# Kernel optimization log

Measured on AMD Instinct MI355X. Metric: run time of the kernel, lower is better.

## Reference

```python
import jax, jax.numpy as jnp
import numpy as np

N, D = 8192, 1024
Q = 4096
DK = 512
DV = 256


def setup_inputs() -> dict:
    key = jax.random.key(0)
    k1, k2, k3, k4, k5, k6 = jax.random.split(key, 6)
    return {
        "search_x": jax.random.normal(k1, (N, D), dtype=jnp.float32),
        "search_y": jax.random.normal(k2, (N, DV), dtype=jnp.float32),
        "query_x": jax.random.normal(k3, (Q, D), dtype=jnp.float32),
        "mask": jax.random.randint(k4, (Q, N), 0, 2, dtype=jnp.int64),
        "Wk": jax.random.normal(k5, (D, DK), dtype=jnp.float32) / np.sqrt(D),
        "Wq": jax.random.normal(k6, (D, DK), dtype=jnp.float32) / np.sqrt(D),
    }


def reference(search_x, search_y, query_x, mask, Wk, Wq):
    # key/query modules: bias-free linear projections (n_keys == 1 after _ensure_key_shape)
    keys = search_x @ Wk            # [N, DK]
    qk = query_x @ Wq               # [Q, DK]
    scale = 1.0 / jnp.sqrt(jnp.asarray(DK, dtype=keys.dtype))
    logits = (qk @ keys.T) * scale  # [Q, N]  (== broadcast mul+sum in original)
    # masked softmax over the search dimension (dim=1)
    m = mask > 0                    # [Q, N]
    neg = jnp.finfo(logits.dtype).min
    p = jax.nn.softmax(jnp.where(m, logits, neg), axis=1)
    p = jnp.where(m, p, 0.0)
    # values = noop_value_module(search_x, search_y) = search_y  [N, DV]
    res = p @ search_y              # [Q, DV]
    return res[:, None, :]          # [Q, n_keys=1, DV], matching original output shape
```

## Files before the change

### kernel.cpp

```cpp
#include <hip/hip_runtime.h>
#include <hip/hip_fp16.h>

typedef _Float16 half4v __attribute__((ext_vector_type(4)));
typedef _Float16 half8v __attribute__((ext_vector_type(8)));
typedef float floatx4 __attribute__((ext_vector_type(4)));

#define GLOBAL_AS __attribute__((address_space(1)))
#define LDS_AS __attribute__((address_space(3)))

__device__ __forceinline__ void async_copy16(const _Float16* g, _Float16* l) {
    __builtin_amdgcn_global_load_lds((const GLOBAL_AS unsigned int*)g,
                                     (LDS_AS unsigned int*)l, 16, 0, 0);
}

template <int R>
__device__ __forceinline__ void stage_tile(const _Float16* g, long ldg,
                                           _Float16* lds, int wave, int lane) {
    const int rl = lane >> 3;
    const int gc = (lane & 7) ^ rl;
#pragma unroll
    for (int i = 0; i < (R >> 5); ++i) {
        const int br = wave * (R >> 2) + i * 8;
        async_copy16(g + (long)(br + rl) * ldg + gc * 8, lds + br * 64);
    }
}

__device__ __forceinline__ void tr_tile(const float* __restrict__ in,
                                        _Float16* __restrict__ out, int R, int C,
                                        int br, int bc, int tid, float (*tile)[33]) {
    int tx = tid & 31, ty = tid >> 5;
#pragma unroll
    for (int i = 0; i < 32; i += 8)
        tile[ty + i][tx] = in[(size_t)(br + ty + i) * C + bc + tx];
    __syncthreads();
#pragma unroll
    for (int i = 0; i < 32; i += 8)
        out[(size_t)(bc + ty + i) * R + br + tx] = (_Float16)tile[tx][ty + i];
    __syncthreads();
}

__global__ __launch_bounds__(256) void k_prep(
    const float* __restrict__ search_x, const float* __restrict__ search_y,
    const float* __restrict__ query_x, const int* __restrict__ mask,
    const float* __restrict__ Wk, const float* __restrict__ Wq,
    _Float16* __restrict__ xh, _Float16* __restrict__ qh,
    _Float16* __restrict__ wkT, _Float16* __restrict__ wqT,
    _Float16* __restrict__ yT, unsigned int* __restrict__ bm) {
    __shared__ float tile[32][33];
    const int bx = blockIdx.x, tid = threadIdx.x;
    if (bx < 2048) {
        const int gw = bx * 4 + (tid >> 6);
        const int lane = tid & 63;
        for (int it = 0; it < 64; ++it) {
            const int idx = (gw * 64 + it) * 64 + lane;
            const int v = mask[idx];
            unsigned long long b = __ballot(v > 0);
            if (lane == 0) bm[idx >> 5] = (unsigned int)b;
            if (lane == 32) bm[idx >> 5] = (unsigned int)(b >> 32);
        }
    } else if (bx < 2560) {
        const int base0 = (bx - 2048) * 256 + tid;
        for (int it = 0; it < 16; ++it) {
            const int i = (it * 512 * 256 + base0) * 4;
            float4 v = *(const float4*)(search_x + i);
            half4v h; h[0]=(_Float16)v.x; h[1]=(_Float16)v.y; h[2]=(_Float16)v.z; h[3]=(_Float16)v.w;
            *(half4v*)(xh + i) = h;
        }
    } else if (bx < 2816) {
        const int base0 = (bx - 2560) * 256 + tid;
        for (int it = 0; it < 16; ++it) {
            const int i = (it * 256 * 256 + base0) * 4;
            float4 v = *(const float4*)(query_x + i);
            half4v h; h[0]=(_Float16)v.x; h[1]=(_Float16)v.y; h[2]=(_Float16)v.z; h[3]=(_Float16)v.w;
            *(half4v*)(qh + i) = h;
        }
    } else if (bx < 2944) {
        for (int it = 0; it < 16; ++it) {
            const int t = (bx - 2816) * 16 + it;
            tr_tile(search_y, yT, 8192, 256, (t >> 3) * 32, (t & 7) * 32, tid, tile);
        }
    } else if (bx < 2976) {
        for (int it = 0; it < 16; ++it) {
            const int t = (bx - 2944) * 16 + it;
            tr_tile(Wk, wkT, 1024, 512, (t >> 4) * 32, (t & 15) * 32, tid, tile);
        }
    } else {
        for (int it = 0; it < 16; ++it) {
            const int t = (bx - 2976) * 16 + it;
            tr_tile(Wq, wqT, 1024, 512, (t >> 4) * 32, (t & 15) * 32, tid, tile);
        }
    }
}

__global__ __launch_bounds__(256, 2) void k_proj(const _Float16* __restrict__ xh,
                                                 const _Float16* __restrict__ qh,
                                                 const _Float16* __restrict__ wkT,
                                                 const _Float16* __restrict__ wqT,
                                                 _Float16* __restrict__ keys,
                                                 _Float16* __restrict__ qk) {
    __shared__ __align__(16) _Float16 As[2][128 * 64];
    __shared__ __align__(16) _Float16 Bs[2][128 * 64];
    const int tid = threadIdx.x, lane = tid & 63, wave = tid >> 6;
    const int wm = (wave >> 1) * 64, wn = (wave & 1) * 64;
    const int quad = lane >> 4, lr = lane & 15;
    const bool isK = blockIdx.y < 64;
    const _Float16* A = isK ? xh : qh;
    const _Float16* B = isK ? wkT : wqT;
    _Float16* C = isK ? keys : qk;
    const long m0 = (long)(isK ? blockIdx.y : blockIdx.y - 64) * 128;
    const long n0 = (long)blockIdx.x * 128;

    floatx4 acc[4][4] = {};
    stage_tile<128>(A + m0 * 1024, 1024, As[0], wave, lane);
    stage_tile<128>(B + n0 * 1024, 1024, Bs[0], wave, lane);
    for (int ktI = 0; ktI < 16; ++ktI) {
        __syncthreads();
        const int cb = ktI & 1;
        if (ktI < 15) {
            stage_tile<128>(A + m0 * 1024 + (ktI + 1) * 64, 1024, As[cb ^ 1], wave, lane);
            stage_tile<128>(B + n0 * 1024 + (ktI + 1) * 64, 1024, Bs[cb ^ 1], wave, lane);
        }
#pragma unroll
        for (int kk = 0; kk < 64; kk += 32) {
            const int sl = ((((kk >> 3) + quad) ^ (lr & 7)) * 8);
            half8v af[4], bf[4];
#pragma unroll
            for (int i = 0; i < 4; ++i) af[i] = *(const half8v*)&As[cb][(wm + i * 16 + lr) * 64 + sl];
#pragma unroll
            for (int j = 0; j < 4; ++j) bf[j] = *(const half8v*)&Bs[cb][(wn + j * 16 + lr) * 64 + sl];
#pragma unroll
            for (int i = 0; i < 4; ++i)
#pragma unroll
                for (int j = 0; j < 4; ++j)
                    acc[i][j] = __builtin_amdgcn_mfma_f32_16x16x32_f16(af[i], bf[j], acc[i][j], 0, 0, 0);
        }
    }
#pragma unroll
    for (int i = 0; i < 4; ++i) {
        long rbase = m0 + wm + i * 16 + quad * 4;
#pragma unroll
        for (int j = 0; j < 4; ++j) {
            long col = n0 + wn + j * 16 + lr;
#pragma unroll
            for (int r = 0; r < 4; ++r)
                C[(rbase + r) * 512 + col] = (_Float16)acc[i][j][r];
        }
    }
}

template <int OUT_MODE>
__global__ __launch_bounds__(256) void k_gemm_nt(const _Float16* __restrict__ A,
                                                 const _Float16* __restrict__ B,
                                                 void* __restrict__ C,
                                                 int M, int N, int K, int kChunk,
                                                 float scale) {
    __shared__ __align__(16) _Float16 As[128 * 64];
    __shared__ __align__(16) _Float16 Bs[128 * 64];
    const int tid = threadIdx.x, lane = tid & 63, wave = tid >> 6;
    const int wm = (wave >> 1) * 64, wn = (wave & 1) * 64;
    const int quad = lane >> 4, lr = lane & 15;
    const long m0 = (long)blockIdx.y * 128, n0 = (long)blockIdx.x * 128;
    const int kBegin = blockIdx.z * kChunk;
    const int kEnd   = kBegin + kChunk;

    floatx4 acc[4][4] = {};
    for (int kt = kBegin; kt < kEnd; kt += 64) {
        stage_tile<128>(A + m0 * K + kt, K, As, wave, lane);
        stage_tile<128>(B + n0 * K + kt, K, Bs, wave, lane);
        __syncthreads();
#pragma unroll
        for (int kk = 0; kk < 64; kk += 32) {
            const int sl = ((((kk >> 3) + quad) ^ (lr & 7)) * 8);
            half8v af[4], bf[4];
#pragma unroll
            for (int i = 0; i < 4; ++i) af[i] = *(const half8v*)&As[(wm + i * 16 + lr) * 64 + sl];
#pragma unroll
            for (int j = 0; j < 4; ++j) bf[j] = *(const half8v*)&Bs[(wn + j * 16 + lr) * 64 + sl];
#pragma unroll
            for (int i = 0; i < 4; ++i)
#pragma unroll
                for (int j = 0; j < 4; ++j)
                    acc[i][j] = __builtin_amdgcn_mfma_f32_16x16x32_f16(af[i], bf[j], acc[i][j], 0, 0, 0);
        }
        __syncthreads();
    }
#pragma unroll
    for (int i = 0; i < 4; ++i) {
        long rbase = m0 + wm + i * 16 + quad * 4;
#pragma unroll
        for (int j = 0; j < 4; ++j) {
            long col = n0 + wn + j * 16 + lr;
#pragma unroll
            for (int r = 0; r < 4; ++r) {
                float val = acc[i][j][r] * scale;
                if (OUT_MODE == 0)
                    ((_Float16*)C)[(rbase + r) * (long)N + col] = (_Float16)val;
                else
                    ((float*)C)[(size_t)blockIdx.z * M * N + (rbase + r) * (long)N + col] = val;
            }
        }
    }
}

__global__ __launch_bounds__(256) void k_softmax(_Float16* __restrict__ logits,
                                                 const unsigned int* __restrict__ bm) {
    const int q   = blockIdx.x;
    const int tid = threadIdx.x;
    _Float16* row = logits + (size_t)q * 8192;
    const unsigned int* bmr = bm + (size_t)q * 256;

    float v[32];
    unsigned mb = 0;
    float lmax = -3.0e38f;
#pragma unroll
    for (int i = 0; i < 8; ++i) {
        int base = i * 1024 + tid * 4;
        half4v h = *(const half4v*)(row + base);
        unsigned bits = (bmr[base >> 5] >> ((tid & 7) * 4)) & 0xFu;
#pragma unroll
        for (int j = 0; j < 4; ++j) {
            v[i * 4 + j] = (float)h[j];
            if ((bits >> j) & 1u) {
                mb |= 1u << (i * 4 + j);
                lmax = fmaxf(lmax, v[i * 4 + j]);
            }
        }
    }
#pragma unroll
    for (int off = 32; off > 0; off >>= 1) lmax = fmaxf(lmax, __shfl_xor(lmax, off, 64));
    __shared__ float redmax[4], redsum[4];
    if ((tid & 63) == 0) redmax[tid >> 6] = lmax;
    __syncthreads();
    lmax = fmaxf(fmaxf(redmax[0], redmax[1]), fmaxf(redmax[2], redmax[3]));

    float lsum = 0.f;
#pragma unroll
    for (int i = 0; i < 32; ++i) {
        float e = ((mb >> i) & 1u) ? __expf(v[i] - lmax) : 0.f;
        v[i] = e;
        lsum += e;
    }
#pragma unroll
    for (int off = 32; off > 0; off >>= 1) lsum += __shfl_xor(lsum, off, 64);
    if ((tid & 63) == 0) redsum[tid >> 6] = lsum;
    __syncthreads();
    lsum = redsum[0] + redsum[1] + redsum[2] + redsum[3];
    float inv = lsum > 0.f ? 1.f / lsum : 0.f;

#pragma unroll
    for (int i = 0; i < 8; ++i) {
        int base = i * 1024 + tid * 4;
        half4v h;
#pragma unroll
        for (int j = 0; j < 4; ++j) h[j] = (_Float16)(v[i * 4 + j] * inv);
        *(half4v*)(row + base) = h;
    }
}

__global__ __launch_bounds__(256) void k_reduce8(const float* __restrict__ part,
                                                 float* __restrict__ out, int n) {
    int i = (blockIdx.x * 256 + threadIdx.x) * 4;
    if (i >= n) return;
    float4 s = *(const float4*)(part + i);
#pragma unroll
    for (int z = 1; z < 8; ++z) {
        float4 v = *(const float4*)(part + (size_t)z * n + i);
        s.x += v.x; s.y += v.y; s.z += v.z; s.w += v.w;
    }
    *(float4*)(out + i) = s;
}

extern "C" void kernel_launch(void* const* d_in, const int* in_sizes, int n_in,
                              void* d_out, int out_size, void* d_ws, size_t ws_size,
                              hipStream_t stream) {
    const float* search_x = (const float*)d_in[0];
    const float* search_y = (const float*)d_in[1];
    const float* query_x  = (const float*)d_in[2];
    const int*   mask     = (const int*)d_in[3];
    const float* Wk       = (const float*)d_in[4];
    const float* Wq       = (const float*)d_in[5];
    (void)in_sizes; (void)n_in; (void)ws_size; (void)out_size;

    char* p = (char*)d_ws;
    _Float16* xh   = (_Float16*)p; p += (size_t)8192 * 1024 * 2;
    _Float16* qh   = (_Float16*)p; p += (size_t)4096 * 1024 * 2;
    _Float16* wkT  = (_Float16*)p; p += (size_t)512 * 1024 * 2;
    _Float16* wqT  = (_Float16*)p; p += (size_t)512 * 1024 * 2;
    _Float16* yT   = (_Float16*)p; p += (size_t)256 * 8192 * 2;
    _Float16* keys = (_Float16*)p; p += (size_t)8192 * 512 * 2;
    _Float16* qk   = (_Float16*)p; p += (size_t)4096 * 512 * 2;
    unsigned int* bmw = (unsigned int*)p; p += (size_t)4096 * 256 * 4;
    _Float16* lg   = (_Float16*)p; p += (size_t)4096 * 8192 * 2;
    float*    part = (float*)p;    p += (size_t)8 * 4096 * 256 * 4;

    k_prep<<<3008, 256, 0, stream>>>(search_x, search_y, query_x, mask, Wk, Wq,
                                     xh, qh, wkT, wqT, yT, bmw);
    k_proj<<<dim3(4, 96), 256, 0, stream>>>(xh, qh, wkT, wqT, keys, qk);
    k_gemm_nt<0><<<dim3(64, 32, 1), 256, 0, stream>>>(qk, keys, lg, 4096, 8192, 512, 512,
                                                      0.04419417382415922f);
    k_softmax<<<4096, 256, 0, stream>>>(lg, bmw);
    k_gemm_nt<1><<<dim3(2, 32, 8), 256, 0, stream>>>(lg, yT, part, 4096, 256, 8192, 1024, 1.0f);
    k_reduce8<<<1024, 256, 0, stream>>>(part, (float*)d_out, 4096 * 256);
}
```

Measured before the change: 414.5 us.

## Fuse mask application into logits GEMM epilogue and widen prep transposes

Drops the separate mask-to-bitmask pass from the prep kernel. The logits GEMM epilogue now reads the int mask directly and writes the half-precision minimum for masked entries, so the softmax no longer needs mask bits. Masked elements then underflow to zero in the exponential instead of being skipped explicitly. The weight and search_y transposes also move to 64x64 tiles with float4 loads and 16-byte half stores, and k_prep launches fewer blocks. The epilogue's mask loads are only partly coalesced. A fully masked row would now give a uniform distribution rather than zeros.

After: 370.3 us. 1.12x faster.

```diff
diff --git a/kernel.cpp b/kernel.cpp
--- a/kernel.cpp
+++ b/kernel.cpp
@@ -25,69 +25,62 @@
     }
 }
 
-__device__ __forceinline__ void tr_tile(const float* __restrict__ in,
-                                        _Float16* __restrict__ out, int R, int C,
-                                        int br, int bc, int tid, float (*tile)[33]) {
-    int tx = tid & 31, ty = tid >> 5;
-#pragma unroll
-    for (int i = 0; i < 32; i += 8)
-        tile[ty + i][tx] = in[(size_t)(br + ty + i) * C + bc + tx];
+__device__ __forceinline__ void tr64(const float* __restrict__ in,
+                                     _Float16* __restrict__ out, int R, int C,
+                                     int br, int bc, int tid, float (*t)[64]) {
+    const int row = tid >> 4;
+    const int col = (tid & 15) * 4;
+#pragma unroll
+    for (int rr = 0; rr < 64; rr += 16) {
+        float4 v = *(const float4*)(in + (size_t)(br + row + rr) * C + bc + col);
+        t[row + rr][col] = v.x; t[row + rr][col + 1] = v.y;
+        t[row + rr][col + 2] = v.z; t[row + rr][col + 3] = v.w;
+    }
     __syncthreads();
-#pragma unroll
-    for (int i = 0; i < 32; i += 8)
-        out[(size_t)(bc + ty + i) * R + br + tx] = (_Float16)tile[tx][ty + i];
-    __syncthreads();
+    const int c  = tid >> 2;
+    const int q4 = (tid & 3) * 16;
+    half8v h0, h1;
+#pragma unroll
+    for (int k = 0; k < 8; ++k) h0[k] = (_Float16)t[q4 + k][c];
+#pragma unroll
+    for (int k = 0; k < 8; ++k) h1[k] = (_Float16)t[q4 + 8 + k][c];
+    *(half8v*)(out + (size_t)(bc + c) * R + br + q4) = h0;
+    *(half8v*)(out + (size_t)(bc + c) * R + br + q4 + 8) = h1;
 }
 
 __global__ __launch_bounds__(256) void k_prep(
     const float* __restrict__ search_x, const float* __restrict__ search_y,
-    const float* __restrict__ query_x, const int* __restrict__ mask,
+    const float* __restrict__ query_x,
     const float* __restrict__ Wk, const float* __restrict__ Wq,
     _Float16* __restrict__ xh, _Float16* __restrict__ qh,
     _Float16* __restrict__ wkT, _Float16* __restrict__ wqT,
-    _Float16* __restrict__ yT, unsigned int* __restrict__ bm) {
-    __shared__ float tile[32][33];
+    _Float16* __restrict__ yT) {
+    __shared__ float tile[64][64];
     const int bx = blockIdx.x, tid = threadIdx.x;
-    if (bx < 2048) {
-        const int gw = bx * 4 + (tid >> 6);
-        const int lane = tid & 63;
-        for (int it = 0; it < 64; ++it) {
-            const int idx = (gw * 64 + it) * 64 + lane;
-            const int v = mask[idx];
-            unsigned long long b = __ballot(v > 0);
-            if (lane == 0) bm[idx >> 5] = (unsigned int)b;
-            if (lane == 32) bm[idx >> 5] = (unsigned int)(b >> 32);
-        }
-    } else if (bx < 2560) {
-        const int base0 = (bx - 2048) * 256 + tid;
+    if (bx < 512) {
+        const int t = bx;
+        tr64(search_y, yT, 8192, 256, (t >> 2) * 64, (t & 3) * 64, tid, tile);
+    } else if (bx < 640) {
+        const int t = bx - 512;
+        tr64(Wk, wkT, 1024, 512, (t >> 3) * 64, (t & 7) * 64, tid, tile);
+    } else if (bx < 768) {
+        const int t = bx - 640;
+        tr64(Wq, wqT, 1024, 512, (t >> 3) * 64, (t & 7) * 64, tid, tile);
+    } else if (bx < 1280) {
+        const int base0 = (bx - 768) * 256 + tid;
         for (int it = 0; it < 16; ++it) {
             const int i = (it * 512 * 256 + base0) * 4;
             float4 v = *(const float4*)(search_x + i);
             half4v h; h[0]=(_Float16)v.x; h[1]=(_Float16)v.y; h[2]=(_Float16)v.z; h[3]=(_Float16)v.w;
             *(half4v*)(xh + i) = h;
         }
-    } else if (bx < 2816) {
-        const int base0 = (bx - 2560) * 256 + tid;
+    } else {
+        const int base0 = (bx - 1280) * 256 + tid;
         for (int it = 0; it < 16; ++it) {
             const int i = (it * 256 * 256 + base0) * 4;
             float4 v = *(const float4*)(query_x + i);
             half4v h; h[0]=(_Float16)v.x; h[1]=(_Float16)v.y; h[2]=(_Float16)v.z; h[3]=(_Float16)v.w;
             *(half4v*)(qh + i) = h;
-        }
-    } else if (bx < 2944) {
-        for (int it = 0; it < 16; ++it) {
-            const int t = (bx - 2816) * 16 + it;
-            tr_tile(search_y, yT, 8192, 256, (t >> 3) * 32, (t & 7) * 32, tid, tile);
-        }
-    } else if (bx < 2976) {
-        for (int it = 0; it < 16; ++it) {
-            const int t = (bx - 2944) * 16 + it;
-            tr_tile(Wk, wkT, 1024, 512, (t >> 4) * 32, (t & 15) * 32, tid, tile);
-        }
-    } else {
-        for (int it = 0; it < 16; ++it) {
-            const int t = (bx - 2976) * 16 + it;
-            tr_tile(Wq, wqT, 1024, 512, (t >> 4) * 32, (t & 15) * 32, tid, tile);
         }
     }
 }
@@ -152,6 +145,7 @@
 __global__ __launch_bounds__(256) void k_gemm_nt(const _Float16* __restrict__ A,
                                                  const _Float16* __restrict__ B,
                                                  void* __restrict__ C,
+                                                 const int* __restrict__ mask,
                                                  int M, int N, int K, int kChunk,
                                                  float scale) {
     __shared__ __align__(16) _Float16 As[128 * 64];
@@ -193,37 +187,33 @@
 #pragma unroll
             for (int r = 0; r < 4; ++r) {
                 float val = acc[i][j][r] * scale;
-                if (OUT_MODE == 0)
-                    ((_Float16*)C)[(rbase + r) * (long)N + col] = (_Float16)val;
-                else
+                if (OUT_MODE == 2) {
+                    const int mk = mask[(rbase + r) * 8192L + col];
+                    ((_Float16*)C)[(rbase + r) * (long)N + col] =
+                        (mk > 0) ? (_Float16)val : (_Float16)(-65504.f);
+                } else {
                     ((float*)C)[(size_t)blockIdx.z * M * N + (rbase + r) * (long)N + col] = val;
+                }
             }
         }
     }
 }
 
-__global__ __launch_bounds__(256) void k_softmax(_Float16* __restrict__ logits,
-                                                 const unsigned int* __restrict__ bm) {
+__global__ __launch_bounds__(256) void k_softmax(_Float16* __restrict__ logits) {
     const int q   = blockIdx.x;
     const int tid = threadIdx.x;
     _Float16* row = logits + (size_t)q * 8192;
-    const unsigned int* bmr = bm + (size_t)q * 256;
 
     float v[32];
-    unsigned mb = 0;
     float lmax = -3.0e38f;
 #pragma unroll
     for (int i = 0; i < 8; ++i) {
         int base = i * 1024 + tid * 4;
         half4v h = *(const half4v*)(row + base);
-        unsigned bits = (bmr[base >> 5] >> ((tid & 7) * 4)) & 0xFu;
 #pragma unroll
         for (int j = 0; j < 4; ++j) {
             v[i * 4 + j] = (float)h[j];
-            if ((bits >> j) & 1u) {
-                mb |= 1u << (i * 4 + j);
-                lmax = fmaxf(lmax, v[i * 4 + j]);
-            }
+            lmax = fmaxf(lmax, v[i * 4 + j]);
         }
     }
 #pragma unroll
@@ -236,7 +226,7 @@
     float lsum = 0.f;
 #pragma unroll
     for (int i = 0; i < 32; ++i) {
-        float e = ((mb >> i) & 1u) ? __expf(v[i] - lmax) : 0.f;
+        float e = __expf(v[i] - lmax);
         v[i] = e;
         lsum += e;
     }
@@ -289,16 +279,15 @@
     _Float16* yT   = (_Float16*)p; p += (size_t)256 * 8192 * 2;
     _Float16* keys = (_Float16*)p; p += (size_t)8192 * 512 * 2;
     _Float16* qk   = (_Float16*)p; p += (size_t)4096 * 512 * 2;
-    unsigned int* bmw = (unsigned int*)p; p += (size_t)4096 * 256 * 4;
     _Float16* lg   = (_Float16*)p; p += (size_t)4096 * 8192 * 2;
     float*    part = (float*)p;    p += (size_t)8 * 4096 * 256 * 4;
 
-    k_prep<<<3008, 256, 0, stream>>>(search_x, search_y, query_x, mask, Wk, Wq,
-                                     xh, qh, wkT, wqT, yT, bmw);
+    k_prep<<<1536, 256, 0, stream>>>(search_x, search_y, query_x, Wk, Wq,
+                                     xh, qh, wkT, wqT, yT);
     k_proj<<<dim3(4, 96), 256, 0, stream>>>(xh, qh, wkT, wqT, keys, qk);
-    k_gemm_nt<0><<<dim3(64, 32, 1), 256, 0, stream>>>(qk, keys, lg, 4096, 8192, 512, 512,
+    k_gemm_nt<2><<<dim3(64, 32, 1), 256, 0, stream>>>(qk, keys, lg, mask, 4096, 8192, 512, 512,
                                                       0.04419417382415922f);
-    k_softmax<<<4096, 256, 0, stream>>>(lg, bmw);
-    k_gemm_nt<1><<<dim3(2, 32, 8), 256, 0, stream>>>(lg, yT, part, 4096, 256, 8192, 1024, 1.0f);
+    k_softmax<<<4096, 256, 0, stream>>>(lg);
+    k_gemm_nt<1><<<dim3(2, 32, 8), 256, 0, stream>>>(lg, yT, part, nullptr, 4096, 256, 8192, 1024, 1.0f);
     k_reduce8<<<1024, 256, 0, stream>>>(part, (float*)d_out, 4096 * 256);
 }
```
